# Performance work log

Hardware: AMD Instinct MI355X
Metric: run time of the kernel (lower is better)

The kernel has to match this reference:

```python
import jax, jax.numpy as jnp
import numpy as np

DIM = 1024
G = 256            # group_size
QK = 128           # query_key_dim
HID = 2048         # int(dim * expansion_factor)
NUM_BUCKETS = 32
MAX_DIST = 128
BIAS_SCALE = QK ** 0.5
LN_EPS = 1e-5


def t5_rel_bias(rel_table):
    # causal T5 relative position bias for a [G, G] block
    pos = jnp.arange(G)
    rel = pos[None, :] - pos[:, None]          # k_pos - q_pos
    n = jnp.maximum(-rel, 0)                   # causal clamp
    max_exact = NUM_BUCKETS // 2               # 16
    is_small = n < max_exact
    ln_ratio = np.log(MAX_DIST / max_exact)
    val_large = max_exact + (
        jnp.log(jnp.maximum(n, 1).astype(jnp.float32) / max_exact) / ln_ratio
        * (NUM_BUCKETS - max_exact)
    ).astype(jnp.int32)
    val_large = jnp.minimum(val_large, NUM_BUCKETS - 1)
    bucket = jnp.where(is_small, n, val_large)
    return rel_table[bucket] * BIAS_SCALE      # [G, G]


def setup_inputs() -> dict:
    key = jax.random.key(0)
    ks = jax.random.split(key, 10)
    s = 0.02
    return {
        "x": jax.random.normal(ks[0], (4, 4096, DIM), dtype=jnp.float32),
        "ln_w": jnp.ones((DIM,), jnp.float32),
        "ln_b": jnp.zeros((DIM,), jnp.float32),
        "Wh": jax.random.normal(ks[1], (DIM, 2 * HID), jnp.float32) * s,
        "bh": jnp.zeros((2 * HID,), jnp.float32),
        "Wqk": jax.random.normal(ks[2], (DIM, QK), jnp.float32) * s,
        "bqk": jnp.zeros((QK,), jnp.float32),
        "qk_w": jax.random.normal(ks[3], (4, QK), jnp.float32) * s + 1.0,
        "qk_b": jnp.zeros((4, QK), jnp.float32),
        "rel_table": jax.random.normal(ks[4], (NUM_BUCKETS,), jnp.float32) * s,
        "Wout": jax.random.normal(ks[5], (HID, DIM), jnp.float32) * s,
        "bout": jnp.zeros((DIM,), jnp.float32),
    }


def reference(x, ln_w, ln_b, Wh, bh, Wqk, bqk, qk_w, qk_b, rel_table, Wout, bout):
    b, n, _ = x.shape
    g = G
    ng = n // g

    # LayerNorm
    mu = jnp.mean(x, -1, keepdims=True)
    var = jnp.var(x, -1, keepdims=True)
    normed = (x - mu) * jax.lax.rsqrt(var + LN_EPS) * ln_w + ln_b

    # projections
    hv = jax.nn.silu(normed @ Wh + bh)
    v, gate = jnp.split(hv, 2, axis=-1)                 # [b, n, HID] each
    qk = jax.nn.silu(normed @ Wqk + bqk)                # [b, n, QK]

    # offset-scale into 4 heads
    qk4 = qk[..., None, :] * qk_w + qk_b                # [b, n, 4, QK]
    quad_q, lin_q, quad_k, lin_k = [qk4[..., h, :] for h in range(4)]

    # group: b (g n) d -> b g n d
    grp = lambda t: t.reshape(b, ng, g, t.shape[-1])
    quad_q, quad_k, lin_q, lin_k, vg = map(grp, (quad_q, quad_k, lin_q, lin_k, v))

    # quadratic branch: ReLU^2 attention with T5 bias, causal within group
    sim = jnp.einsum('bgid,bgjd->bgij', quad_q, quad_k) / g
    sim = sim + t5_rel_bias(rel_table)
    attn = jnp.square(jax.nn.relu(sim))
    causal_mask = jnp.triu(jnp.ones((g, g), bool), 1)
    attn = jnp.where(causal_mask, 0.0, attn)
    quad_out = jnp.einsum('bgij,bgje->bgie', attn, vg)  # [b, ng, g, HID]

    # linear branch: per-group kv summary, causal via shifted cumsum over groups
    lin_kv = jnp.einsum('bgnd,bgne->bgde', lin_k, vg) / g   # [b, ng, QK, HID]
    lin_kv = jnp.cumsum(lin_kv, axis=1)
    lin_kv = jnp.pad(lin_kv, ((0, 0), (1, 0), (0, 0), (0, 0)))[:, :-1]
    lin_out = jnp.einsum('bgde,bgnd->bgne', lin_kv, lin_q)  # [b, ng, g, HID]

    out = gate * (quad_out + lin_out).reshape(b, n, HID)
    return out @ Wout + bout + x
```

## Files before the change

### kernel.cpp

```cpp
#include <hip/hip_runtime.h>
#include <hip/hip_bf16.h>

typedef unsigned short u16;
typedef short s8v __attribute__((ext_vector_type(8)));
typedef float f4v __attribute__((ext_vector_type(4)));

__device__ __forceinline__ float b2f(u16 u) { return __uint_as_float(((unsigned)u) << 16); }
__device__ __forceinline__ u16 f2b(float f) {
    unsigned u = __float_as_uint(f);
    unsigned r = 0x7FFFu + ((u >> 16) & 1u);
    return (u16)((u + r) >> 16);
}
__device__ __forceinline__ float silu_f(float x) { return x / (1.0f + expf(-x)); }

__device__ __forceinline__ void gld16(const u16* g, u16* l) {
    __builtin_amdgcn_global_load_lds((const __attribute__((address_space(1))) unsigned*)g,
                                     (__attribute__((address_space(3))) unsigned*)l, 16, 0, 0);
}

__device__ __forceinline__ void mfma_block(const u16* Al, const u16* Bl, f4v acc[4][4],
                                           int wr, int wc, int l15, int quad, int l7) {
#pragma unroll
    for (int ks = 0; ks < 2; ++ks) {
        s8v af[4], bf[4];
        int cch = ((ks * 4 + quad) ^ l7) * 8;
#pragma unroll
        for (int mi = 0; mi < 4; ++mi)
            af[mi] = *(const s8v*)(Al + (wr * 64 + mi * 16 + l15) * 64 + cch);
#pragma unroll
        for (int ni = 0; ni < 4; ++ni)
            bf[ni] = *(const s8v*)(Bl + (wc * 64 + ni * 16 + l15) * 64 + cch);
#pragma unroll
        for (int mi = 0; mi < 4; ++mi)
#pragma unroll
            for (int ni = 0; ni < 4; ++ni)
                acc[mi][ni] = __builtin_amdgcn_mfma_f32_16x16x32_bf16(af[mi], bf[ni], acc[mi][ni], 0, 0, 0);
    }
}

__device__ __forceinline__ void stage_plane(const u16* __restrict__ src, int K, int kbase,
                                            u16* dst, int t) {
    const int row = t >> 2, ch = t & 3;
    const int csw = (ch ^ (row & 3) ^ ((row >> 2) & 3)) * 8;
    gld16(src + (size_t)row * K + kbase + csw, dst + row * 32 + ch * 8);
    gld16(src + (size_t)(row + 128) * K + kbase + csw, dst + (row + 128) * 32 + ch * 8);
}

__device__ __forceinline__ void read_frag4(const u16* plane, s8v (&f)[4], int rbase, int l15, int quad) {
#pragma unroll
    for (int mi = 0; mi < 4; ++mi) {
        int r = rbase + mi * 16 + l15;
        f[mi] = *(const s8v*)(plane + r * 32 + ((quad ^ (r & 3) ^ ((r >> 2) & 3)) * 8));
    }
}

__device__ __forceinline__ void mfma_quad(f4v (&a4)[4][4], const s8v (&af)[4], const s8v (&bf)[4]) {
    __builtin_amdgcn_s_setprio(1);
#pragma unroll
    for (int mi = 0; mi < 4; ++mi)
#pragma unroll
        for (int ni = 0; ni < 4; ++ni)
            a4[mi][ni] = __builtin_amdgcn_mfma_f32_16x16x32_bf16(af[mi], bf[ni], a4[mi][ni], 0, 0, 0);
    __builtin_amdgcn_s_setprio(0);
}

__device__ __forceinline__ void kloop2ph(const u16* __restrict__ Ag, const u16* __restrict__ Bg,
                                         int K, int NT, u16* lds8, f4v (&acc)[8][4],
                                         int t, int wm, int wn, int l15, int quad) {
#pragma unroll
    for (int T = 0; T < 3; ++T) {
        u16* Ab = lds8 + T * 16384;
        stage_plane(Ag, K, T * 32, Ab, t);
        stage_plane(Bg, K, T * 32, Ab + 8192, t);
    }
    asm volatile("s_waitcnt vmcnt(8)" ::: "memory");
    __builtin_amdgcn_s_barrier();

    s8v bf[4];
    for (int T = 0; T < NT; ++T) {
        const u16* Ab = lds8 + (T & 3) * 16384;
        const u16* Bb = Ab + 8192;
        u16* Sb = lds8 + ((T + 3) & 3) * 16384;
        const bool st = (T < NT - 3);
        s8v af[4];
        read_frag4(Bb, bf, wn * 64, l15, quad);
        read_frag4(Ab, af, wm * 128, l15, quad);
        if (st) stage_plane(Ag, K, (T + 3) * 32, Sb, t);
        __builtin_amdgcn_s_setprio(1);
#pragma unroll
        for (int mi = 0; mi < 4; ++mi)
#pragma unroll
            for (int ni = 0; ni < 4; ++ni)
                acc[mi][ni] = __builtin_amdgcn_mfma_f32_16x16x32_bf16(af[mi], bf[ni], acc[mi][ni], 0, 0, 0);
        __builtin_amdgcn_s_setprio(0);
        __builtin_amdgcn_s_barrier();
        read_frag4(Ab, af, wm * 128 + 64, l15, quad);
        if (st) stage_plane(Bg, K, (T + 3) * 32, Sb + 8192, t);
        __builtin_amdgcn_s_setprio(1);
#pragma unroll
        for (int mi = 0; mi < 4; ++mi)
#pragma unroll
            for (int ni = 0; ni < 4; ++ni)
                acc[4 + mi][ni] = __builtin_amdgcn_mfma_f32_16x16x32_bf16(af[mi], bf[ni], acc[4 + mi][ni], 0, 0, 0);
        __builtin_amdgcn_s_setprio(0);
        if (T < NT - 3)       asm volatile("s_waitcnt vmcnt(8)" ::: "memory");
        else if (T == NT - 3) asm volatile("s_waitcnt vmcnt(4)" ::: "memory");
        else if (T == NT - 2) asm volatile("s_waitcnt vmcnt(0)" ::: "memory");
        __builtin_amdgcn_s_barrier();
    }
}

__device__ __forceinline__ void kloop8(const u16* __restrict__ Ag, const u16* __restrict__ Bg,
                                       int K, int NT, u16* lds, f4v (&acc)[2][4][4],
                                       int t, int wm, int wn, int l15, int quad) {
    stage_plane(Ag, K, 0,  lds, t);
    stage_plane(Bg, K, 0,  lds + 16384, t);
    stage_plane(Ag, K, 32, lds + 8192, t);
    stage_plane(Bg, K, 32, lds + 24576, t);
    stage_plane(Ag, K, 64, lds + 32768, t);
    stage_plane(Bg, K, 64, lds + 32768 + 16384, t);
    asm volatile("s_waitcnt vmcnt(4)" ::: "memory");
    __builtin_amdgcn_s_barrier();

    const int ab0 = wm * 128, ab1 = wm * 128 + 64, bb = wn * 64;
    s8v af[4], bf[4];
    for (int j = 0; j < NT; ++j) {
        u16* cur = lds + (j & 1) * 32768;
        u16* nxt = lds + ((j + 1) & 1) * 32768;
        const u16* Ak0 = cur;
        const u16* Ak1 = cur + 8192;
        const u16* Bk0 = cur + 16384;
        const u16* Bk1 = cur + 24576;
        const bool s1 = (j + 1 < NT), s2 = (j + 2 < NT);

        read_frag4(Bk0, bf, bb, l15, quad);
        read_frag4(Ak0, af, ab0, l15, quad);
        if (s1) stage_plane(Ag, K, (j + 1) * 64 + 32, nxt + 8192, t);
        __builtin_amdgcn_s_barrier();
        mfma_quad(acc[0], af, bf);
        __builtin_amdgcn_s_barrier();
        read_frag4(Ak0, af, ab1, l15, quad);
        if (s1) stage_plane(Bg, K, (j + 1) * 64 + 32, nxt + 24576, t);
        __builtin_amdgcn_s_barrier();
        mfma_quad(acc[1], af, bf);
        __builtin_amdgcn_s_barrier();
        read_frag4(Bk1, bf, bb, l15, quad);
        read_frag4(Ak1, af, ab0, l15, quad);
        if (s2) stage_plane(Ag, K, (j + 2) * 64, cur, t);
        __builtin_amdgcn_s_barrier();
        mfma_quad(acc[0], af, bf);
        __builtin_amdgcn_s_barrier();
        read_frag4(Ak1, af, ab1, l15, quad);
        if (s2) stage_plane(Bg, K, (j + 2) * 64, cur + 16384, t);
        if (j < NT - 2) asm volatile("s_waitcnt vmcnt(4)" ::: "memory");
        else            asm volatile("s_waitcnt vmcnt(0)" ::: "memory");
        __builtin_amdgcn_s_barrier();
        mfma_quad(acc[1], af, bf);
        __builtin_amdgcn_s_barrier();
    }
}


__global__ __launch_bounds__(256) void convT_kernel(const float* __restrict__ in,
                                                    u16* __restrict__ out, int K, int N) {
    __shared__ float tile[32][33];
    int k0 = blockIdx.y * 32, n0 = blockIdx.x * 32;
    int t = threadIdx.x;
    int r = t >> 5, c = t & 31;
#pragma unroll
    for (int rr = r; rr < 32; rr += 8) tile[rr][c] = in[(size_t)(k0 + rr) * N + n0 + c];
    __syncthreads();
#pragma unroll
    for (int rr = r; rr < 32; rr += 8) out[(size_t)(n0 + rr) * K + k0 + c] = f2b(tile[c][rr]);
}

__global__ __launch_bounds__(256) void ln_kernel(const float* __restrict__ x,
                                                 const float* __restrict__ w,
                                                 const float* __restrict__ bsh,
                                                 u16* __restrict__ out) {
    int row = blockIdx.x, t = threadIdx.x;
    const float* xr = x + (size_t)row * 1024;
    float4 u = *reinterpret_cast<const float4*>(xr + t * 4);
    float s = u.x + u.y + u.z + u.w;
    float s2 = u.x * u.x + u.y * u.y + u.z * u.z + u.w * u.w;
#pragma unroll
    for (int o = 32; o; o >>= 1) {
        s += __shfl_down(s, o, 64);
        s2 += __shfl_down(s2, o, 64);
    }
    __shared__ float rs[4], rs2[4];
    int wid = t >> 6;
    if ((t & 63) == 0) { rs[wid] = s; rs2[wid] = s2; }
    __syncthreads();
    float S = rs[0] + rs[1] + rs[2] + rs[3];
    float S2 = rs2[0] + rs2[1] + rs2[2] + rs2[3];
    float mu = S * (1.0f / 1024.0f);
    float var = S2 * (1.0f / 1024.0f) - mu * mu;
    float rinv = rsqrtf(var + 1e-5f);
    float4 uw = *reinterpret_cast<const float4*>(w + t * 4);
    float4 ub = *reinterpret_cast<const float4*>(bsh + t * 4);
    ushort4 o;
    o.x = f2b((u.x - mu) * rinv * uw.x + ub.x);
    o.y = f2b((u.y - mu) * rinv * uw.y + ub.y);
    o.z = f2b((u.z - mu) * rinv * uw.z + ub.z);
    o.w = f2b((u.w - mu) * rinv * uw.w + ub.w);
    *reinterpret_cast<ushort4*>(out + (size_t)row * 1024 + t * 4) = o;
}

__global__ __launch_bounds__(512) void gemm_hv256(const u16* __restrict__ A,
                                                  const u16* __restrict__ Bt,
                                                  const float* __restrict__ bias,
                                                  u16* __restrict__ vT,
                                                  u16* __restrict__ gate) {
    __shared__ __align__(16) u16 lds8[65536];
    const int t = threadIdx.x;
    const int lane = t & 63, w = t >> 6;
    const int wm = w >> 2, wn = w & 3;
    const int l15 = lane & 15, quad = lane >> 4;

    int wg = blockIdx.x;
    wg = (wg & 7) * 128 + (wg >> 3);
    const int by = wg >> 4, bx = wg & 15;
    const int m0 = by * 256, n0 = bx * 256;

    f4v acc[2][4][4] = {};
    kloop8(A + (size_t)m0 * 1024, Bt + (size_t)n0 * 1024, 1024, 16,
           lds8, acc, t, wm, wn, l15, quad);

    const bool isV = (n0 < 2048);
    const int bg = by;
#pragma unroll
    for (int ni = 0; ni < 4; ++ni) {
        int n = n0 + wn * 64 + ni * 16 + l15;
        float bs = bias[n];
#pragma unroll
        for (int mg = 0; mg < 2; ++mg) {
#pragma unroll
            for (int m = 0; m < 4; ++m) {
                int mloc = wm * 128 + (mg * 4 + m) * 16 + quad * 4;
                if (isV) {
                    ushort4 o;
                    o.x = f2b(silu_f(acc[mg][m][ni][0] + bs));
                    o.y = f2b(silu_f(acc[mg][m][ni][1] + bs));
                    o.z = f2b(silu_f(acc[mg][m][ni][2] + bs));
                    o.w = f2b(silu_f(acc[mg][m][ni][3] + bs));
                    *reinterpret_cast<ushort4*>(vT + ((size_t)bg * 2048 + n) * 256 + mloc) = o;
                } else {
#pragma unroll
                    for (int reg = 0; reg < 4; ++reg)
                        gate[(size_t)(m0 + mloc + reg) * 2048 + (n - 2048)] =
                            f2b(silu_f(acc[mg][m][ni][reg] + bs));
                }
            }
        }
    }
}

__global__ __launch_bounds__(512) void gemm_out256(const u16* __restrict__ A,
                                                   const u16* __restrict__ Bt,
                                                   const float* __restrict__ bias,
                                                   const float* __restrict__ resid,
                                                   float* __restrict__ C) {
    __shared__ __align__(16) u16 lds8[65536];
    const int t = threadIdx.x;
    const int lane = t & 63, w = t >> 6;
    const int wm = w >> 2, wn = w & 3;
    const int l15 = lane & 15, quad = lane >> 4;

    int wg = blockIdx.x;
    wg = (wg & 7) * 32 + (wg >> 3);
    const int by = wg >> 2, bx = wg & 3;
    const int m0 = by * 256, n0 = bx * 256;

    f4v acc[8][4] = {};
    kloop2ph(A + (size_t)m0 * 2048, Bt + (size_t)n0 * 2048, 2048, 64,
             lds8, acc, t, wm, wn, l15, quad);

#pragma unroll
    for (int ni = 0; ni < 4; ++ni) {
        int n = n0 + wn * 64 + ni * 16 + l15;
        float bs = bias[n];
#pragma unroll
        for (int mi = 0; mi < 8; ++mi) {
#pragma unroll
            for (int reg = 0; reg < 4; ++reg) {
                int m = m0 + wm * 128 + mi * 16 + quad * 4 + reg;
                C[(size_t)m * 1024 + n] = acc[mi][ni][reg] + bs + resid[(size_t)m * 1024 + n];
            }
        }
    }
}

__global__ __launch_bounds__(256) void gemm_qk(const u16* __restrict__ A,
                                               const u16* __restrict__ Bt,
                                               const float* __restrict__ bias,
                                               u16* __restrict__ C) {
    __shared__ __align__(16) u16 Al[128 * 64];
    __shared__ __align__(16) u16 Bl[128 * 64];
    const int t = threadIdx.x;
    const int lane = t & 63, w = t >> 6;
    const int wr = w >> 1, wc = w & 1;
    const int l15 = lane & 15, quad = lane >> 4, l7 = lane & 7;
    const int m0 = blockIdx.y * 128;
    const int sr = t >> 3, ss = t & 7;

    f4v acc[4][4] = {};
    for (int k0 = 0; k0 < 1024; k0 += 64) {
#pragma unroll
        for (int i = 0; i < 4; ++i) {
            int r = i * 32 + sr;
            int q = ss ^ (r & 7);
            gld16(A + (size_t)(m0 + r) * 1024 + q * 8 + k0, Al + i * 2048 + t * 8);
            gld16(Bt + (size_t)r * 1024 + q * 8 + k0, Bl + i * 2048 + t * 8);
        }
        __syncthreads();
        mfma_block(Al, Bl, acc, wr, wc, l15, quad, l7);
        __syncthreads();
    }
#pragma unroll
    for (int ni = 0; ni < 4; ++ni) {
        int n = wc * 64 + ni * 16 + l15;
        float bs = bias[n];
#pragma unroll
        for (int mi = 0; mi < 4; ++mi) {
#pragma unroll
            for (int reg = 0; reg < 4; ++reg) {
                int m = m0 + wr * 64 + mi * 16 + quad * 4 + reg;
                C[(size_t)m * 128 + n] = f2b(silu_f(acc[mi][ni][reg] + bs));
            }
        }
    }
}

__global__ __launch_bounds__(256) void klT_kernel(const u16* __restrict__ qk,
                                                  const float* __restrict__ qk_w,
                                                  const float* __restrict__ qk_b,
                                                  u16* __restrict__ klT) {
    __shared__ __align__(16) u16 tile[64][128];
    const int bg = blockIdx.x >> 2, jc = (blockIdx.x & 3) * 64;
    const int t = threadIdx.x;
    const int r = t >> 4, c = (t & 15) * 8;
#pragma unroll
    for (int rr = 0; rr < 64; rr += 16)
        *(s8v*)(&tile[r + rr][c]) =
            *(const s8v*)(qk + (size_t)(bg * 256 + jc + r + rr) * 128 + c);
    __syncthreads();
    const int d = t & 127, jb = (t >> 7) * 32;
    const float kw = qk_w[3 * 128 + d], kb = qk_b[3 * 128 + d];
    s8v ov[4];
#pragma unroll
    for (int q = 0; q < 4; ++q)
#pragma unroll
        for (int j = 0; j < 8; ++j)
            ov[q][j] = (short)f2b(b2f(tile[jb + q * 8 + j][d]) * kw + kb);
    u16* dst = klT + ((size_t)bg * 128 + d) * 256 + jc + jb;
#pragma unroll
    for (int q = 0; q < 4; ++q) *(s8v*)(dst + q * 8) = ov[q];
}

__global__ __launch_bounds__(256) void scores_kernel(const u16* __restrict__ qk,
                                                     const float* __restrict__ qk_w,
                                                     const float* __restrict__ qk_b,
                                                     const float* __restrict__ rel_table,
                                                     u16* __restrict__ Sbuf) {
    __shared__ __align__(16) u16 qkl[256 * 128];
    __shared__ float biasn[256];
    __shared__ float w0[128], b0[128], w1[128], b1[128], w2[128], b2v[128];
    const int t = threadIdx.x;
    const int bg = blockIdx.x >> 1, mt = blockIdx.x & 1;
    const int lane = t & 63, w = t >> 6;
    const int wr = w >> 1, wc = w & 1;
    const int l15 = lane & 15, quad = lane >> 4;

    if (t < 128) {
        w0[t] = qk_w[t];        b0[t] = qk_b[t];
        w1[t] = qk_w[128 + t];  b1[t] = qk_b[128 + t];
        w2[t] = qk_w[256 + t];  b2v[t] = qk_b[256 + t];
    }
    {
        int n = t;
        int bucket;
        if (n < 16) bucket = n;
        else {
            float v = logf((float)n / 16.0f) / 2.0794415416798357f * 16.0f;
            int vl = 16 + (int)v;
            bucket = vl > 31 ? 31 : vl;
        }
        biasn[n] = rel_table[bucket] * 11.313708498984761f;
    }
#pragma unroll
    for (int it = 0; it < 16; ++it) {
        int r = (t >> 4) + it * 16, c = (t & 15) * 8;
        *(s8v*)(qkl + r * 128 + c) = *(const s8v*)(qk + ((size_t)(bg * 256 + r)) * 128 + c);
    }
    __syncthreads();

    f4v acc[4][8] = {};
#pragma unroll
    for (int kstep = 0; kstep < 4; ++kstep) {
        int kc = kstep * 32 + quad * 8;
        float w0f[8], b0f[8], w2f[8], b2f_[8];
#pragma unroll
        for (int j = 0; j < 8; ++j) {
            w0f[j] = w0[kc + j]; b0f[j] = b0[kc + j];
            w2f[j] = w2[kc + j]; b2f_[j] = b2v[kc + j];
        }
        s8v af[4];
#pragma unroll
        for (int mi = 0; mi < 4; ++mi) {
            int ra = mt * 128 + wr * 64 + mi * 16 + l15;
            s8v raw = *(const s8v*)(qkl + ra * 128 + kc);
#pragma unroll
            for (int j = 0; j < 8; ++j) af[mi][j] = (short)f2b(b2f((u16)raw[j]) * w0f[j] + b0f[j]);
        }
#pragma unroll
        for (int np = 0; np < 2; ++np) {
            s8v bf[4];
#pragma unroll
            for (int ni = 0; ni < 4; ++ni) {
                int rb = wc * 128 + (np * 4 + ni) * 16 + l15;
                s8v raw = *(const s8v*)(qkl + rb * 128 + kc);
#pragma unroll
                for (int j = 0; j < 8; ++j) bf[ni][j] = (short)f2b(b2f((u16)raw[j]) * w2f[j] + b2f_[j]);
            }
#pragma unroll
            for (int mi = 0; mi < 4; ++mi)
#pragma unroll
                for (int ni = 0; ni < 4; ++ni)
                    acc[mi][np * 4 + ni] = __builtin_amdgcn_mfma_f32_16x16x32_bf16(af[mi], bf[ni], acc[mi][np * 4 + ni], 0, 0, 0);
        }
    }
#pragma unroll
    for (int ni = 0; ni < 8; ++ni) {
        int gj = wc * 128 + ni * 16 + l15;
#pragma unroll
        for (int mi = 0; mi < 4; ++mi) {
#pragma unroll
            for (int reg = 0; reg < 4; ++reg) {
                int gi = mt * 128 + wr * 64 + mi * 16 + quad * 4 + reg;
                float aval = 0.0f;
                if (gj <= gi) {
                    float sv = acc[mi][ni][reg] * (1.0f / 256.0f) + biasn[gi - gj];
                    sv = fmaxf(sv, 0.0f);
                    aval = sv * sv;
                }
                Sbuf[((size_t)bg * 256 + gi) * 384 + gj] = f2b(aval);
            }
        }
    }
#pragma unroll
    for (int it = 0; it < 8; ++it) {
        int i = mt * 128 + (t >> 4) + it * 16;
        int d = (t & 15) * 8;
        s8v raw = *(const s8v*)(qkl + i * 128 + d);
        u16* dst = Sbuf + ((size_t)bg * 256 + i) * 384 + 256 + d;
#pragma unroll
        for (int j = 0; j < 8; ++j)
            dst[j] = f2b(b2f((u16)raw[j]) * w1[d + j] + b1[d + j]);
    }
}

__global__ __launch_bounds__(256) void kv_gemm(const u16* __restrict__ vT,
                                               const u16* __restrict__ klT,
                                               u16* __restrict__ kvT) {
    __shared__ __align__(16) u16 Al[128 * 64];
    __shared__ __align__(16) u16 Bl[128 * 64];
    const int t = threadIdx.x;
    const int lane = t & 63, w = t >> 6;
    const int wr = w >> 1, wc = w & 1;
    const int l15 = lane & 15, quad = lane >> 4, l7 = lane & 7;
    const int bg = blockIdx.y, m0 = blockIdx.x * 128;
    const int sr = t >> 3, ss = t & 7;

    const u16* Av = vT + (size_t)bg * 2048 * 256;
    const u16* Bk = klT + (size_t)bg * 128 * 256;

    f4v acc[4][4] = {};
    for (int k0 = 0; k0 < 256; k0 += 64) {
#pragma unroll
        for (int i = 0; i < 4; ++i) {
            int r = i * 32 + sr;
            int q = ss ^ (r & 7);
            gld16(Av + (size_t)(m0 + r) * 256 + q * 8 + k0, Al + i * 2048 + t * 8);
            gld16(Bk + (size_t)r * 256 + q * 8 + k0, Bl + i * 2048 + t * 8);
        }
        __syncthreads();
        mfma_block(Al, Bl, acc, wr, wc, l15, quad, l7);
        __syncthreads();
    }
#pragma unroll
    for (int ni = 0; ni < 4; ++ni) {
        int n = wc * 64 + ni * 16 + l15;
#pragma unroll
        for (int mi = 0; mi < 4; ++mi) {
#pragma unroll
            for (int reg = 0; reg < 4; ++reg) {
                int m = m0 + wr * 64 + mi * 16 + quad * 4 + reg;
                kvT[((size_t)bg * 2048 + m) * 128 + n] = f2b(acc[mi][ni][reg] * (1.0f / 256.0f));
            }
        }
    }
}

__global__ __launch_bounds__(256) void prefix_kernel(u16* __restrict__ kvT) {
    size_t tid = (size_t)blockIdx.x * 256 + threadIdx.x;
    int d = (int)(tid & 127);
    int e = (int)((tid >> 7) & 2047);
    int b = (int)(tid >> 18);
    size_t base = ((size_t)(b * 16) * 2048 + e) * 128 + d;
    const size_t gs = 2048 * 128;
    float vals[16];
#pragma unroll
    for (int g = 0; g < 16; ++g) vals[g] = b2f(kvT[base + (size_t)g * gs]);
    float s = 0.0f;
#pragma unroll
    for (int g = 0; g < 16; ++g) {
        kvT[base + (size_t)g * gs] = f2b(s);
        s += vals[g];
    }
}

__global__ __launch_bounds__(256) void attn_gemm(const u16* __restrict__ Sbuf,
                                                 const u16* __restrict__ vT,
                                                 const u16* __restrict__ kvT,
                                                 u16* __restrict__ gate) {
    __shared__ __align__(16) u16 Al[128 * 64];
    __shared__ __align__(16) u16 Bl[128 * 64];
    const int t = threadIdx.x;
    const int lane = t & 63, w = t >> 6;
    const int wr = w >> 1, wc = w & 1;
    const int l15 = lane & 15, quad = lane >> 4, l7 = lane & 7;
    const int bg = blockIdx.y >> 1, mt = blockIdx.y & 1;
    const int n0 = blockIdx.x * 128;
    const int sr = t >> 3, ss = t & 7;

    const u16* Abase = Sbuf + ((size_t)bg * 256 + mt * 128) * 384;
    const u16* Bv = vT + (size_t)bg * 2048 * 256;
    const u16* Bk = kvT + (size_t)bg * 2048 * 128;

    f4v acc[4][4] = {};
    for (int k0 = 0; k0 < 256; k0 += 64) {
#pragma unroll
        for (int i = 0; i < 4; ++i) {
            int r = i * 32 + sr;
            int q = ss ^ (r & 7);
            gld16(Abase + (size_t)r * 384 + q * 8 + k0, Al + i * 2048 + t * 8);
            gld16(Bv + (size_t)(n0 + r) * 256 + q * 8 + k0, Bl + i * 2048 + t * 8);
        }
        __syncthreads();
        mfma_block(Al, Bl, acc, wr, wc, l15, quad, l7);
        __syncthreads();
    }
    for (int k0 = 0; k0 < 128; k0 += 64) {
#pragma unroll
        for (int i = 0; i < 4; ++i) {
            int r = i * 32 + sr;
            int q = ss ^ (r & 7);
            gld16(Abase + (size_t)r * 384 + 256 + q * 8 + k0, Al + i * 2048 + t * 8);
            gld16(Bk + (size_t)(n0 + r) * 128 + q * 8 + k0, Bl + i * 2048 + t * 8);
        }
        __syncthreads();
        mfma_block(Al, Bl, acc, wr, wc, l15, quad, l7);
        __syncthreads();
    }
#pragma unroll
    for (int ni = 0; ni < 4; ++ni) {
        int e = n0 + wc * 64 + ni * 16 + l15;
#pragma unroll
        for (int mi = 0; mi < 4; ++mi) {
#pragma unroll
            for (int reg = 0; reg < 4; ++reg) {
                int gi = mt * 128 + wr * 64 + mi * 16 + quad * 4 + reg;
                u16* p = gate + ((size_t)bg * 256 + gi) * 2048 + e;
                *p = f2b(acc[mi][ni][reg] * b2f(*p));
            }
        }
    }
}

extern "C" void kernel_launch(void* const* d_in, const int* in_sizes, int n_in,
                              void* d_out, int out_size, void* d_ws, size_t ws_size,
                              hipStream_t stream) {
    const float* x = (const float*)d_in[0];
    const float* ln_w = (const float*)d_in[1];
    const float* ln_b = (const float*)d_in[2];
    const float* Wh = (const float*)d_in[3];
    const float* bh = (const float*)d_in[4];
    const float* Wqk = (const float*)d_in[5];
    const float* bqk = (const float*)d_in[6];
    const float* qk_w = (const float*)d_in[7];
    const float* qk_b = (const float*)d_in[8];
    const float* rel_table = (const float*)d_in[9];
    const float* Wout = (const float*)d_in[10];
    const float* bout = (const float*)d_in[11];
    float* out = (float*)d_out;

    char* ws = (char*)d_ws;
    u16* normed = (u16*)(ws);
    u16* kvT    = (u16*)(ws);
    u16* gate   = (u16*)(ws + 33554432ull);
    u16* vT     = (u16*)(ws + 100663296ull);
    u16* qk     = (u16*)(ws + 167772160ull);
    u16* WhT    = (u16*)(ws + 171966464ull);
    u16* klT    = (u16*)(ws + 171966464ull);
    u16* WoutT  = (u16*)(ws + 180355072ull);
    u16* Sbuf   = (u16*)(ws + 184549376ull);
    u16* WqkT   = (u16*)(ws + 184549376ull);

    convT_kernel<<<dim3(128, 32), 256, 0, stream>>>(Wh, WhT, 1024, 4096);
    convT_kernel<<<dim3(32, 64), 256, 0, stream>>>(Wout, WoutT, 2048, 1024);
    convT_kernel<<<dim3(4, 32), 256, 0, stream>>>(Wqk, WqkT, 1024, 128);
    ln_kernel<<<16384, 256, 0, stream>>>(x, ln_w, ln_b, normed);
    gemm_hv256<<<1024, 512, 0, stream>>>(normed, WhT, bh, vT, gate);
    gemm_qk<<<dim3(1, 128), 256, 0, stream>>>(normed, WqkT, bqk, qk);
    klT_kernel<<<256, 256, 0, stream>>>(qk, qk_w, qk_b, klT);
    scores_kernel<<<128, 256, 0, stream>>>(qk, qk_w, qk_b, rel_table, Sbuf);
    kv_gemm<<<dim3(16, 64), 256, 0, stream>>>(vT, klT, kvT);
    prefix_kernel<<<4096, 256, 0, stream>>>(kvT);
    attn_gemm<<<dim3(16, 128), 256, 0, stream>>>(Sbuf, vT, kvT, gate);
    gemm_out256<<<256, 512, 0, stream>>>(gate, WoutT, bout, x, out);
}
```

Before: 577.5 us.

## Merge weight transposes, fuse klT into gemm_qk, add lgkmcnt waits

The three weight-transpose launches become a single kernel that picks its matrix from the block index. The klT scale/shift/transpose kernel is folded into the gemm_qk epilogue, which now writes klT directly with scattered 2-byte stores. This saves two launches and one read of qk. Explicit lgkmcnt(0) waits are also placed before each MFMA quad in the pipelined GEMM loop. These waits may make LDS reads ordering-correct but could serialize latency hiding, and the scattered klT stores are uncoalesced.

```diff
diff --git a/kernel.cpp b/kernel.cpp
--- a/kernel.cpp
+++ b/kernel.cpp
@@ -137,17 +137,20 @@
         read_frag4(Ak0, af, ab0, l15, quad);
         if (s1) stage_plane(Ag, K, (j + 1) * 64 + 32, nxt + 8192, t);
         __builtin_amdgcn_s_barrier();
+        asm volatile("s_waitcnt lgkmcnt(0)" ::: "memory");
         mfma_quad(acc[0], af, bf);
         __builtin_amdgcn_s_barrier();
         read_frag4(Ak0, af, ab1, l15, quad);
         if (s1) stage_plane(Bg, K, (j + 1) * 64 + 32, nxt + 24576, t);
         __builtin_amdgcn_s_barrier();
+        asm volatile("s_waitcnt lgkmcnt(0)" ::: "memory");
         mfma_quad(acc[1], af, bf);
         __builtin_amdgcn_s_barrier();
         read_frag4(Bk1, bf, bb, l15, quad);
         read_frag4(Ak1, af, ab0, l15, quad);
         if (s2) stage_plane(Ag, K, (j + 2) * 64, cur, t);
         __builtin_amdgcn_s_barrier();
+        asm volatile("s_waitcnt lgkmcnt(0)" ::: "memory");
         mfma_quad(acc[0], af, bf);
         __builtin_amdgcn_s_barrier();
         read_frag4(Ak1, af, ab1, l15, quad);
@@ -155,16 +158,26 @@
         if (j < NT - 2) asm volatile("s_waitcnt vmcnt(4)" ::: "memory");
         else            asm volatile("s_waitcnt vmcnt(0)" ::: "memory");
         __builtin_amdgcn_s_barrier();
+        asm volatile("s_waitcnt lgkmcnt(0)" ::: "memory");
         mfma_quad(acc[1], af, bf);
         __builtin_amdgcn_s_barrier();
     }
 }
 
 
-__global__ __launch_bounds__(256) void convT_kernel(const float* __restrict__ in,
-                                                    u16* __restrict__ out, int K, int N) {
+__global__ __launch_bounds__(256) void convT_all(const float* __restrict__ Wh,
+                                                 const float* __restrict__ Wout,
+                                                 const float* __restrict__ Wqk,
+                                                 u16* __restrict__ WhT,
+                                                 u16* __restrict__ WoutT,
+                                                 u16* __restrict__ WqkT) {
     __shared__ float tile[32][33];
-    int k0 = blockIdx.y * 32, n0 = blockIdx.x * 32;
+    int b = blockIdx.x;
+    const float* in; u16* out; int K, N, bx, by;
+    if (b < 4096)      { in = Wh;   out = WhT;   K = 1024; N = 4096; bx = b & 127; by = b >> 7; }
+    else if (b < 6144) { b -= 4096; in = Wout; out = WoutT; K = 2048; N = 1024; bx = b & 31; by = b >> 5; }
+    else               { b -= 6144; in = Wqk;  out = WqkT;  K = 1024; N = 128;  bx = b & 3;  by = b >> 2; }
+    int k0 = by * 32, n0 = bx * 32;
     int t = threadIdx.x;
     int r = t >> 5, c = t & 31;
 #pragma unroll
@@ -294,7 +307,10 @@
 __global__ __launch_bounds__(256) void gemm_qk(const u16* __restrict__ A,
                                                const u16* __restrict__ Bt,
                                                const float* __restrict__ bias,
-                                               u16* __restrict__ C) {
+                                               const float* __restrict__ qk_w,
+                                               const float* __restrict__ qk_b,
+                                               u16* __restrict__ C,
+                                               u16* __restrict__ klT) {
     __shared__ __align__(16) u16 Al[128 * 64];
     __shared__ __align__(16) u16 Bl[128 * 64];
     const int t = threadIdx.x;
@@ -321,41 +337,18 @@
     for (int ni = 0; ni < 4; ++ni) {
         int n = wc * 64 + ni * 16 + l15;
         float bs = bias[n];
+        float kw = qk_w[3 * 128 + n], kb = qk_b[3 * 128 + n];
 #pragma unroll
         for (int mi = 0; mi < 4; ++mi) {
 #pragma unroll
             for (int reg = 0; reg < 4; ++reg) {
                 int m = m0 + wr * 64 + mi * 16 + quad * 4 + reg;
-                C[(size_t)m * 128 + n] = f2b(silu_f(acc[mi][ni][reg] + bs));
+                u16 qv = f2b(silu_f(acc[mi][ni][reg] + bs));
+                C[(size_t)m * 128 + n] = qv;
+                klT[(((size_t)(m >> 8)) * 128 + n) * 256 + (m & 255)] = f2b(b2f(qv) * kw + kb);
             }
         }
     }
-}
-
-__global__ __launch_bounds__(256) void klT_kernel(const u16* __restrict__ qk,
-                                                  const float* __restrict__ qk_w,
-                                                  const float* __restrict__ qk_b,
-                                                  u16* __restrict__ klT) {
-    __shared__ __align__(16) u16 tile[64][128];
-    const int bg = blockIdx.x >> 2, jc = (blockIdx.x & 3) * 64;
-    const int t = threadIdx.x;
-    const int r = t >> 4, c = (t & 15) * 8;
-#pragma unroll
-    for (int rr = 0; rr < 64; rr += 16)
-        *(s8v*)(&tile[r + rr][c]) =
-            *(const s8v*)(qk + (size_t)(bg * 256 + jc + r + rr) * 128 + c);
-    __syncthreads();
-    const int d = t & 127, jb = (t >> 7) * 32;
-    const float kw = qk_w[3 * 128 + d], kb = qk_b[3 * 128 + d];
-    s8v ov[4];
-#pragma unroll
-    for (int q = 0; q < 4; ++q)
-#pragma unroll
-        for (int j = 0; j < 8; ++j)
-            ov[q][j] = (short)f2b(b2f(tile[jb + q * 8 + j][d]) * kw + kb);
-    u16* dst = klT + ((size_t)bg * 128 + d) * 256 + jc + jb;
-#pragma unroll
-    for (int q = 0; q < 4; ++q) *(s8v*)(dst + q * 8) = ov[q];
 }
 
 __global__ __launch_bounds__(256) void scores_kernel(const u16* __restrict__ qk,
@@ -607,13 +600,10 @@
     u16* Sbuf   = (u16*)(ws + 184549376ull);
     u16* WqkT   = (u16*)(ws + 184549376ull);
 
-    convT_kernel<<<dim3(128, 32), 256, 0, stream>>>(Wh, WhT, 1024, 4096);
-    convT_kernel<<<dim3(32, 64), 256, 0, stream>>>(Wout, WoutT, 2048, 1024);
-    convT_kernel<<<dim3(4, 32), 256, 0, stream>>>(Wqk, WqkT, 1024, 128);
+    convT_all<<<6272, 256, 0, stream>>>(Wh, Wout, Wqk, WhT, WoutT, WqkT);
     ln_kernel<<<16384, 256, 0, stream>>>(x, ln_w, ln_b, normed);
     gemm_hv256<<<1024, 512, 0, stream>>>(normed, WhT, bh, vT, gate);
-    gemm_qk<<<dim3(1, 128), 256, 0, stream>>>(normed, WqkT, bqk, qk);
-    klT_kernel<<<256, 256, 0, stream>>>(qk, qk_w, qk_b, klT);
+    gemm_qk<<<dim3(1, 128), 256, 0, stream>>>(normed, WqkT, bqk, qk_w, qk_b, qk, klT);
     scores_kernel<<<128, 256, 0, stream>>>(qk, qk_w, qk_b, rel_table, Sbuf);
     kv_gemm<<<dim3(16, 64), 256, 0, stream>>>(vT, klT, kvT);
     prefix_kernel<<<4096, 256, 0, stream>>>(kvT);
```

Result: no change. 583.8 us (+1.1%).
